# Kernel tuning notes

Hardware: AMD Instinct MI355X
Metric: run time of the kernel (lower is better)

The kernel has to match this reference:

```python
import jax, jax.numpy as jnp
import numpy as np

EPS = 1e-12

def l2_normalize(x, axis=-1):
    # matches torch F.normalize(p=2, dim=1, eps=1e-12) for 2D input
    n = jnp.sqrt(jnp.sum(x * x, axis=axis, keepdims=True))
    return x / jnp.maximum(n, EPS)

def setup_inputs() -> dict:
    key = jax.random.key(0)
    ks = jax.random.split(key, 7)
    N, D = 8192, 256
    s = 1.0 / np.sqrt(D)
    x = jax.random.normal(ks[0], (N, D), dtype=jnp.float32)
    Wq = jax.random.uniform(ks[1], (D, D), jnp.float32, -s, s)
    bq = jax.random.uniform(ks[2], (D,), jnp.float32, -s, s)
    Wk = jax.random.uniform(ks[3], (D, D), jnp.float32, -s, s)
    bk = jax.random.uniform(ks[4], (D,), jnp.float32, -s, s)
    Wv = jax.random.uniform(ks[5], (D, D), jnp.float32, -s, s)
    bv = jax.random.uniform(ks[6], (D,), jnp.float32, -s, s)
    return {"x": x, "Wq": Wq, "bq": bq, "Wk": Wk, "bk": bk, "Wv": Wv, "bv": bv}

def reference(x, Wq, bq, Wk, bk, Wv, bv):
    q = l2_normalize(x @ Wq.T + bq)           # [N, D]
    k = l2_normalize(x @ Wk.T + bk)           # [N, D]
    v = x @ Wv.T + bv                         # [N, D]
    cos_sim = q @ k.T                         # [N, N]
    w = jax.nn.relu(cos_sim)
    # zero diagonal, then renormalize rows to sum 1
    N = w.shape[0]
    w = jnp.where(jnp.eye(N, dtype=bool), 0.0, w)
    w = w / jnp.maximum(jnp.sum(w, axis=-1, keepdims=True), EPS)
    return w @ v + x
```

## Files before the change

kernel.cpp:

```cpp
#include <hip/hip_runtime.h>

#define NROWS 8192
#define DDIM  256
#define KSPLIT 4
#define BM 128
#define BK 64
#define NT (NROWS / KSPLIT / BK)

typedef __bf16 bf16x8 __attribute__((ext_vector_type(8)));
typedef float  f32x4  __attribute__((ext_vector_type(4)));
typedef float  f32x16 __attribute__((ext_vector_type(16)));

typedef __attribute__((address_space(1))) unsigned int uint_gas;
typedef __attribute__((address_space(3))) unsigned int uint_las;

__device__ __forceinline__ void gload_lds16(const void* g, void* l) {
  __builtin_amdgcn_global_load_lds((const uint_gas*)g, (uint_las*)l, 16, 0, 0);
}

__device__ __forceinline__ unsigned int f2bf_bits(float f) {
  union { float f; unsigned int u; } v; v.f = f;
  unsigned int r = v.u + 0x7FFFu + ((v.u >> 16) & 1u);
  return r >> 16;
}
__device__ __forceinline__ float bf2f(unsigned int b) {
  union { unsigned int u; float f; } v; v.u = b << 16;
  return v.f;
}
__device__ __forceinline__ unsigned int pack2bf(float a, float b) {
  union { unsigned int u; __bf16 h[2]; } p;
  p.h[0] = (__bf16)a; p.h[1] = (__bf16)b;
  return p.u;
}
__device__ __forceinline__ unsigned short f2h_bits(float f) {
  union { _Float16 h; unsigned short u; } c; c.h = (_Float16)f;
  return c.u;
}
__device__ __forceinline__ float h2f(unsigned short u) {
  union { unsigned short u; _Float16 h; } c; c.u = u;
  return (float)c.h;
}

#define NXFRAG (512 * 8 * 64)
#define NWFRAG (3 * 16 * 8 * 64)
__global__ __launch_bounds__(256) void convert_kernel(
    const float* __restrict__ x, const float* __restrict__ wq,
    const float* __restrict__ wk, const float* __restrict__ wv,
    unsigned short* __restrict__ xp, unsigned short* __restrict__ Wp)
{
  int tid = blockIdx.x * 256 + threadIdx.x;
  const float* src;
  unsigned short* dst;
  int row, col;
  if (tid < NXFRAG) {
    int l = tid & 63, ks = (tid >> 6) & 7, rt = tid >> 9;
    src = x; dst = xp + (size_t)tid * 8;
    row = rt * 16 + (l & 15); col = ks * 32 + (l >> 4) * 8;
  } else {
    int fid = tid - NXFRAG;
    if (fid >= NWFRAG) return;
    int l = fid & 63, ks = (fid >> 6) & 7, ct = (fid >> 9) & 15, out = fid >> 13;
    src = (out == 0) ? wq : (out == 1) ? wk : wv;
    dst = Wp + (size_t)fid * 8;
    row = ct * 16 + (l & 15); col = ks * 32 + (l >> 4) * 8;
  }
  const float* p = src + (size_t)row * DDIM + col;
  float4 f0 = *(const float4*)p;
  float4 f1 = *(const float4*)(p + 4);
  ushort4 o0, o1;
  o0.x = (unsigned short)f2bf_bits(f0.x); o0.y = (unsigned short)f2bf_bits(f0.y);
  o0.z = (unsigned short)f2bf_bits(f0.z); o0.w = (unsigned short)f2bf_bits(f0.w);
  o1.x = (unsigned short)f2bf_bits(f1.x); o1.y = (unsigned short)f2bf_bits(f1.y);
  o1.z = (unsigned short)f2bf_bits(f1.z); o1.w = (unsigned short)f2bf_bits(f1.w);
  *(ushort4*)dst = o0;
  *(ushort4*)(dst + 4) = o1;
}

__global__ __launch_bounds__(256) void qkv_kernel(
    const float* __restrict__ bq, const float* __restrict__ bk, const float* __restrict__ bv,
    const unsigned short* __restrict__ xp, const unsigned short* __restrict__ Wp,
    unsigned short* __restrict__ qb, unsigned short* __restrict__ kb,
    unsigned short* __restrict__ vtp)
{
  __shared__ unsigned short vstage[DDIM * 72];
  const int t = threadIdx.x;
  const int w = t >> 6, l = t & 63;
  const int c = l & 15, g = l >> 4;
  const int out = blockIdx.x / 128;
  const int mb  = blockIdx.x % 128;
  const int row0 = mb * 64;
  const int rw = row0 + w * 16;
  const int rt = mb * 4 + w;

  bf16x8 a[8];
  #pragma unroll
  for (int ks = 0; ks < 8; ks++)
    a[ks] = *(const bf16x8*)(xp + ((size_t)(rt * 8 + ks) * 64 + l) * 8);

  const float* bias = (out == 0) ? bq : (out == 1) ? bk : bv;
  f32x4 vals[16];
  #pragma unroll
  for (int ct = 0; ct < 16; ct++) {
    f32x4 acc = {0.f, 0.f, 0.f, 0.f};
    #pragma unroll
    for (int ks = 0; ks < 8; ks++) {
      bf16x8 b = *(const bf16x8*)(Wp + ((size_t)((out * 16 + ct) * 8 + ks) * 64 + l) * 8);
      acc = __builtin_amdgcn_mfma_f32_16x16x32_bf16(a[ks], b, acc, 0, 0, 0);
    }
    float bias_v = bias[ct * 16 + c];
    #pragma unroll
    for (int r = 0; r < 4; r++) acc[r] += bias_v;
    vals[ct] = acc;
  }
  if (out < 2) {
    #pragma unroll
    for (int r = 0; r < 4; r++) {
      float ss = 0.f;
      #pragma unroll
      for (int ct = 0; ct < 16; ct++) ss += vals[ct][r] * vals[ct][r];
      ss += __shfl_xor(ss, 1); ss += __shfl_xor(ss, 2);
      ss += __shfl_xor(ss, 4); ss += __shfl_xor(ss, 8);
      float inv = 1.f / fmaxf(sqrtf(ss), 1e-12f);
      #pragma unroll
      for (int ct = 0; ct < 16; ct++) vals[ct][r] *= inv;
    }
    unsigned short* dst = (out == 0) ? qb : kb;
    #pragma unroll
    for (int ct = 0; ct < 16; ct++) {
      #pragma unroll
      for (int r = 0; r < 4; r++) {
        unsigned int bits = f2bf_bits(vals[ct][r]);
        unsigned int ob = (unsigned int)__shfl_xor((int)bits, 1);
        if (!(l & 1))
          *(unsigned int*)(dst + (size_t)(rw + g * 4 + r) * DDIM + ct * 16 + c) =
              bits | (ob << 16);
      }
    }
  } else {
    #pragma unroll
    for (int ct = 0; ct < 16; ct++)
      #pragma unroll
      for (int r = 0; r < 4; r++)
        vstage[(ct * 16 + c) * 72 + (w * 16 + g * 4 + r)] =
            (unsigned short)f2bf_bits(vals[ct][r]);
    __syncthreads();
    unsigned short* wdst = vtp + (size_t)mb * 16384;
    #pragma unroll
    for (int p = 0; p < 8; p++) {
      int n = p * 256 + t;
      int dg = ((n >> 8) << 5) + (n & 31);
      int s  = (n >> 5) & 7;
      *(uint4*)(wdst + (size_t)n * 8) = *(const uint4*)(vstage + dg * 72 + s * 8);
    }
  }
}

__global__ __launch_bounds__(1024, 4) void attn_kernel(
    const unsigned short* __restrict__ qb, const unsigned short* __restrict__ kb,
    const unsigned short* __restrict__ vtp,
    unsigned short* __restrict__ nump, float* __restrict__ denp)
{
  __shared__ __align__(16) char smem[163840];
  char* kbuf = smem;
  char* vbuf = smem + 65536;
  char* Pb   = smem + 131072;

  const int t = threadIdx.x;
  const int w = t >> 6, l = t & 63;
  const int l31 = l & 31, hi = l >> 5;
  const int rw = w & 7;
  const int ts = t & 511;
  const int bid = blockIdx.x;
  const int split = bid & (KSPLIT - 1);
  const int mb = bid >> 2;
  const int q0 = mb * BM;
  const int kbase0 = split * (NROWS / KSPLIT);
  const char* kbc = (const char*)kb;
  const char* vtc = (const char*)vtp;

  if (w < 8) {
    const int sr = rw >> 1, sc = rw & 1;
    const int qrow = sr * 32 + l31;
    const int qrowg = q0 + qrow;
    const int krl = sc * 32 + l31;

    bf16x8 qa[16];
    {
      const unsigned short* qrowp = qb + (size_t)(q0 + qrow) * DDIM + hi * 8;
      #pragma unroll
      for (int m = 0; m < 16; m++) qa[m] = *(const bf16x8*)(qrowp + m * 16);
    }
    float denl = 0.f;

    auto stageK = [&](int buf, int it) {
      const char* ksrc = kbc + (size_t)(kbase0 + it * BK) * 512;
      #pragma unroll
      for (int i = 0; i < 4; i++) {
        int n = i * 512 + ts;
        int row = n >> 5, slot = n & 31;
        gload_lds16(ksrc + row * 512 + (((slot - row) & 31) << 4),
                    kbuf + buf * 32768 + i * 8192 + rw * 1024);
      }
    };

    stageK(0, 0);
    asm volatile("s_waitcnt vmcnt(0)" ::: "memory");
    __builtin_amdgcn_sched_barrier(0);
    __builtin_amdgcn_s_barrier();
    __builtin_amdgcn_sched_barrier(0);

    for (int it = 0; it < NT; ++it) {
      const int cur = it & 1;
      if (it + 1 < NT) stageK(cur ^ 1, it + 1);
      __builtin_amdgcn_sched_barrier(0);

      const char* kcur = kbuf + cur * 32768;
      f32x16 sacc = (f32x16){0.f};
      #pragma unroll
      for (int m = 0; m < 16; m++) {
        bf16x8 kf = *(const bf16x8*)(kcur + krl * 512 +
                                     (((m * 2 + hi + krl) & 31) << 4));
        sacc = __builtin_amdgcn_mfma_f32_32x32x16_bf16(kf, qa[m], sacc, 0, 0, 0);
      }
      char* pbase = Pb + cur * 16384 + sr * 4096 + l31 * 16 + hi * 8;
      const int kbase = kbase0 + it * BK;
      if (__builtin_expect(kbase < q0 + BM && q0 < kbase + BK, 0)) {
        const int dref = qrowg - (kbase + sc * 32 + hi * 4);
        #pragma unroll
        for (int q = 0; q < 4; q++) {
          float v0 = fmaxf(sacc[4 * q + 0], 0.f);
          float v1 = fmaxf(sacc[4 * q + 1], 0.f);
          float v2 = fmaxf(sacc[4 * q + 2], 0.f);
          float v3 = fmaxf(sacc[4 * q + 3], 0.f);
          const int d = dref - 8 * q;
          v0 = (d == 0) ? 0.f : v0;
          v1 = (d == 1) ? 0.f : v1;
          v2 = (d == 2) ? 0.f : v2;
          v3 = (d == 3) ? 0.f : v3;
          denl += (v0 + v1) + (v2 + v3);
          uint2 d2;
          d2.x = pack2bf(v0, v1);
          d2.y = pack2bf(v2, v3);
          *(uint2*)(pbase + (sc * 4 + q) * 512) = d2;
        }
      } else {
        #pragma unroll
        for (int q = 0; q < 4; q++) {
          float v0 = fmaxf(sacc[4 * q + 0], 0.f);
          float v1 = fmaxf(sacc[4 * q + 1], 0.f);
          float v2 = fmaxf(sacc[4 * q + 2], 0.f);
          float v3 = fmaxf(sacc[4 * q + 3], 0.f);
          denl += (v0 + v1) + (v2 + v3);
          uint2 d2;
          d2.x = pack2bf(v0, v1);
          d2.y = pack2bf(v2, v3);
          *(uint2*)(pbase + (sc * 4 + q) * 512) = d2;
        }
      }
      asm volatile("s_waitcnt vmcnt(0) lgkmcnt(0)" ::: "memory");
      __builtin_amdgcn_sched_barrier(0);
      __builtin_amdgcn_s_barrier();
      __builtin_amdgcn_sched_barrier(0);
    }

    float d = denl;
    d += __shfl_xor(d, 32);
    if (l < 32)
      denp[((size_t)split * 2 + sc) * NROWS + q0 + sr * 32 + l] = d;
  } else {
    const int pr = rw >> 2, pc = rw & 3;

    f32x16 oacc[2][2];
    #pragma unroll
    for (int rt = 0; rt < 2; rt++)
      #pragma unroll
      for (int dt = 0; dt < 2; dt++)
        oacc[rt][dt] = (f32x16){0.f};

    auto stageV = [&](int buf, int it) {
      const char* vsrc = vtc + (size_t)((kbase0 + it * BK) >> 6) * 32768;
      #pragma unroll
      for (int i = 0; i < 4; i++) {
        int n = i * 512 + ts;
        gload_lds16(vsrc + n * 16,
                    vbuf + buf * 32768 + i * 8192 + rw * 1024);
      }
    };

    __builtin_amdgcn_s_barrier();
    __builtin_amdgcn_sched_barrier(0);

    for (int it = 0; it < NT; ++it) {
      const int cur = it & 1;
      stageV(cur, it);
      __builtin_amdgcn_sched_barrier(0);

      if (it > 0) {
        const char* Pprev = Pb + (cur ^ 1) * 16384;
        const char* vprev = vbuf + (cur ^ 1) * 32768;
        #pragma unroll
        for (int ch = 0; ch < 4; ch++) {
          const int s512 = (ch * 2 + hi) * 512 + l31 * 16;
          bf16x8 pa0 = *(const bf16x8*)(Pprev + (pr * 2 + 0) * 4096 + s512);
          bf16x8 pa1 = *(const bf16x8*)(Pprev + (pr * 2 + 1) * 4096 + s512);
          #pragma unroll
          for (int dt = 0; dt < 2; dt++) {
            bf16x8 vf = *(const bf16x8*)(vprev + (pc * 2 + dt) * 4096 + s512);
            oacc[0][dt] = __builtin_amdgcn_mfma_f32_32x32x16_bf16(pa0, vf, oacc[0][dt], 0, 0, 0);
            oacc[1][dt] = __builtin_amdgcn_mfma_f32_32x32x16_bf16(pa1, vf, oacc[1][dt], 0, 0, 0);
          }
        }
      }
      asm volatile("s_waitcnt vmcnt(0) lgkmcnt(0)" ::: "memory");
      __builtin_amdgcn_sched_barrier(0);
      __builtin_amdgcn_s_barrier();
      __builtin_amdgcn_sched_barrier(0);
    }

    {
      const int last = (NT - 1) & 1;
      const char* Pprev = Pb + last * 16384;
      const char* vprev = vbuf + last * 32768;
      #pragma unroll
      for (int ch = 0; ch < 4; ch++) {
        const int s512 = (ch * 2 + hi) * 512 + l31 * 16;
        bf16x8 pa0 = *(const bf16x8*)(Pprev + (pr * 2 + 0) * 4096 + s512);
        bf16x8 pa1 = *(const bf16x8*)(Pprev + (pr * 2 + 1) * 4096 + s512);
        #pragma unroll
        for (int dt = 0; dt < 2; dt++) {
          bf16x8 vf = *(const bf16x8*)(vprev + (pc * 2 + dt) * 4096 + s512);
          oacc[0][dt] = __builtin_amdgcn_mfma_f32_32x32x16_bf16(pa0, vf, oacc[0][dt], 0, 0, 0);
          oacc[1][dt] = __builtin_amdgcn_mfma_f32_32x32x16_bf16(pa1, vf, oacc[1][dt], 0, 0, 0);
        }
      }
    }

    unsigned short* np = nump + (size_t)split * NROWS * DDIM;
    #pragma unroll
    for (int rt = 0; rt < 2; rt++)
      #pragma unroll
      for (int dt = 0; dt < 2; dt++)
        #pragma unroll
        for (int r = 0; r < 16; r++) {
          int rowg = q0 + pr * 64 + rt * 32 + (r & 3) + 8 * (r >> 2) + 4 * hi;
          int col  = pc * 64 + dt * 32 + l31;
          np[(size_t)rowg * DDIM + col] = f2h_bits(oacc[rt][dt][r]);
        }
  }
}

__global__ __launch_bounds__(256) void combine_kernel(
    const float* __restrict__ x,
    const unsigned short* __restrict__ nump, const float* __restrict__ denp,
    float* __restrict__ out)
{
  const int t = threadIdx.x;
  const int w = t >> 6, l = t & 63;
  const int i = blockIdx.x * 4 + w;

  float den = 0.f;
  #pragma unroll
  for (int sp = 0; sp < KSPLIT * 2; sp++)
    den += denp[(size_t)sp * NROWS + i];
  float inv = 1.f / fmaxf(den, 1e-12f);

  const int d0 = l * 4;
  float4 acc = {0.f, 0.f, 0.f, 0.f};
  #pragma unroll
  for (int sp = 0; sp < KSPLIT; sp++) {
    ushort4 u4 = *(const ushort4*)(nump + ((size_t)sp * NROWS + i) * DDIM + d0);
    acc.x += h2f(u4.x); acc.y += h2f(u4.y);
    acc.z += h2f(u4.z); acc.w += h2f(u4.w);
  }
  float4 xx = *(const float4*)(x + (size_t)i * DDIM + d0);
  float4 o;
  o.x = acc.x * inv + xx.x;
  o.y = acc.y * inv + xx.y;
  o.z = acc.z * inv + xx.z;
  o.w = acc.w * inv + xx.w;
  *(float4*)(out + (size_t)i * DDIM + d0) = o;
}

extern "C" void kernel_launch(void* const* d_in, const int* in_sizes, int n_in,
                              void* d_out, int out_size, void* d_ws, size_t ws_size,
                              hipStream_t stream)
{
  const float* x  = (const float*)d_in[0];
  const float* Wq = (const float*)d_in[1];
  const float* bq = (const float*)d_in[2];
  const float* Wk = (const float*)d_in[3];
  const float* bk = (const float*)d_in[4];
  const float* Wv = (const float*)d_in[5];
  const float* bv = (const float*)d_in[6];

  char* ws = (char*)d_ws;
  unsigned short* xp   = (unsigned short*)(ws + 0);
  unsigned short* Wp   = (unsigned short*)(ws + 4194304);
  unsigned short* qb   = (unsigned short*)(ws + 4587520);
  unsigned short* kb   = (unsigned short*)(ws + 8781824);
  unsigned short* vtp  = (unsigned short*)(ws + 12976128);
  unsigned short* nump = (unsigned short*)(ws + 17170432);
  float* denp = (float*)(ws + 33947648);

  convert_kernel<<<1120, 256, 0, stream>>>(x, Wq, Wk, Wv, xp, Wp);
  qkv_kernel<<<384, 256, 0, stream>>>(bq, bk, bv, xp, Wp, qb, kb, vtp);
  attn_kernel<<<(NROWS / BM) * KSPLIT, 1024, 0, stream>>>(qb, kb, vtp, nump, denp);
  combine_kernel<<<NROWS / 4, 256, 0, stream>>>(x, nump, denp, (float*)d_out);
}
```

Measured before the change: 122.0 us.

## Load V fragments directly into registers instead of staging through LDS

The PV consumer waves now read their V MFMA operands straight from global memory into double-buffered register arrays, and the LDS V double buffer is removed. This cuts shared memory from 160KB to 96KB and drops the LDS write and read traffic for V. In exchange each wave issues uncached-pattern global loads and holds 16 extra bf16x8 registers. The barrier waits now cover only lgkmcnt, so the register loads rely on the compiler's implicit waits.

```diff
diff --git a/kernel.cpp b/kernel.cpp
--- a/kernel.cpp
+++ b/kernel.cpp
@@ -160,10 +160,9 @@
     const unsigned short* __restrict__ vtp,
     unsigned short* __restrict__ nump, float* __restrict__ denp)
 {
-  __shared__ __align__(16) char smem[163840];
+  __shared__ __align__(16) char smem[98304];
   char* kbuf = smem;
-  char* vbuf = smem + 65536;
-  char* Pb   = smem + 131072;
+  char* Pb   = smem + 65536;
 
   const int t = threadIdx.x;
   const int w = t >> 6, l = t & 63;
@@ -277,50 +276,18 @@
       for (int dt = 0; dt < 2; dt++)
         oacc[rt][dt] = (f32x16){0.f};
 
-    auto stageV = [&](int buf, int it) {
+    bf16x8 vfrA[8], vfrB[8];
+
+    auto loadV = [&](bf16x8 (&dst)[8], int it) {
       const char* vsrc = vtc + (size_t)((kbase0 + it * BK) >> 6) * 32768;
       #pragma unroll
-      for (int i = 0; i < 4; i++) {
-        int n = i * 512 + ts;
-        gload_lds16(vsrc + n * 16,
-                    vbuf + buf * 32768 + i * 8192 + rw * 1024);
-      }
+      for (int ch = 0; ch < 4; ch++)
+        #pragma unroll
+        for (int dt = 0; dt < 2; dt++)
+          dst[ch * 2 + dt] = *(const bf16x8*)(vsrc + (pc * 2 + dt) * 4096 +
+                                              (ch * 2 + hi) * 512 + l31 * 16);
     };
-
-    __builtin_amdgcn_s_barrier();
-    __builtin_amdgcn_sched_barrier(0);
-
-    for (int it = 0; it < NT; ++it) {
-      const int cur = it & 1;
-      stageV(cur, it);
-      __builtin_amdgcn_sched_barrier(0);
-
-      if (it > 0) {
-        const char* Pprev = Pb + (cur ^ 1) * 16384;
-        const char* vprev = vbuf + (cur ^ 1) * 32768;
-        #pragma unroll
-        for (int ch = 0; ch < 4; ch++) {
-          const int s512 = (ch * 2 + hi) * 512 + l31 * 16;
-          bf16x8 pa0 = *(const bf16x8*)(Pprev + (pr * 2 + 0) * 4096 + s512);
-          bf16x8 pa1 = *(const bf16x8*)(Pprev + (pr * 2 + 1) * 4096 + s512);
-          #pragma unroll
-          for (int dt = 0; dt < 2; dt++) {
-            bf16x8 vf = *(const bf16x8*)(vprev + (pc * 2 + dt) * 4096 + s512);
-            oacc[0][dt] = __builtin_amdgcn_mfma_f32_32x32x16_bf16(pa0, vf, oacc[0][dt], 0, 0, 0);
-            oacc[1][dt] = __builtin_amdgcn_mfma_f32_32x32x16_bf16(pa1, vf, oacc[1][dt], 0, 0, 0);
-          }
-        }
-      }
-      asm volatile("s_waitcnt vmcnt(0) lgkmcnt(0)" ::: "memory");
-      __builtin_amdgcn_sched_barrier(0);
-      __builtin_amdgcn_s_barrier();
-      __builtin_amdgcn_sched_barrier(0);
-    }
-
-    {
-      const int last = (NT - 1) & 1;
-      const char* Pprev = Pb + last * 16384;
-      const char* vprev = vbuf + last * 32768;
+    auto pvcomp = [&](const bf16x8 (&vfr)[8], const char* Pprev) {
       #pragma unroll
       for (int ch = 0; ch < 4; ch++) {
         const int s512 = (ch * 2 + hi) * 512 + l31 * 16;
@@ -328,12 +295,32 @@
         bf16x8 pa1 = *(const bf16x8*)(Pprev + (pr * 2 + 1) * 4096 + s512);
         #pragma unroll
         for (int dt = 0; dt < 2; dt++) {
-          bf16x8 vf = *(const bf16x8*)(vprev + (pc * 2 + dt) * 4096 + s512);
-          oacc[0][dt] = __builtin_amdgcn_mfma_f32_32x32x16_bf16(pa0, vf, oacc[0][dt], 0, 0, 0);
-          oacc[1][dt] = __builtin_amdgcn_mfma_f32_32x32x16_bf16(pa1, vf, oacc[1][dt], 0, 0, 0);
+          oacc[0][dt] = __builtin_amdgcn_mfma_f32_32x32x16_bf16(pa0, vfr[ch * 2 + dt],
+                                                                oacc[0][dt], 0, 0, 0);
+          oacc[1][dt] = __builtin_amdgcn_mfma_f32_32x32x16_bf16(pa1, vfr[ch * 2 + dt],
+                                                                oacc[1][dt], 0, 0, 0);
         }
       }
-    }
+    };
+
+    __builtin_amdgcn_s_barrier();
+    __builtin_amdgcn_sched_barrier(0);
+
+    for (int it2 = 0; it2 < NT; it2 += 2) {
+      loadV(vfrA, it2);
+      if (it2 > 0) pvcomp(vfrB, Pb + 16384);
+      asm volatile("s_waitcnt lgkmcnt(0)" ::: "memory");
+      __builtin_amdgcn_sched_barrier(0);
+      __builtin_amdgcn_s_barrier();
+      __builtin_amdgcn_sched_barrier(0);
+      loadV(vfrB, it2 + 1);
+      pvcomp(vfrA, Pb + 0);
+      asm volatile("s_waitcnt lgkmcnt(0)" ::: "memory");
+      __builtin_amdgcn_sched_barrier(0);
+      __builtin_amdgcn_s_barrier();
+      __builtin_amdgcn_sched_barrier(0);
+    }
+    pvcomp(vfrB, Pb + 16384);
 
     unsigned short* np = nump + (size_t)split * NROWS * DDIM;
     #pragma unroll
```

New measurement: 122.2 us (median of 3 runs). About the same (+0.1%).
